# Optimization experiments

Measured on AMD Instinct MI355X. Metric: run time of the kernel, lower is better.

Reference implementation:

```python
import jax, jax.numpy as jnp
import numpy as np

V = 50257      # output vocab size
EMB = 1024     # embedding_size
HD = 1024      # decoder_hidden_size
HE = 1024      # encoder_hidden_size
L = 128        # max_src_length
B = 64         # batch_size
SCALE = 0.02


def setup_inputs() -> dict:
    key = jax.random.key(0)
    ks = jax.random.split(key, 16)
    inp = {
        "input_tensor": jax.random.randint(ks[0], (1, B), 0, V),
        "hidden": jax.random.normal(ks[1], (1, B, HD), dtype=jnp.float32),
        "encoder_outputs": jax.random.normal(ks[2], (L, B, HE), dtype=jnp.float32),
        "batch_size": B,
        # parameters
        "emb_table": jax.random.normal(ks[3], (V, EMB), dtype=jnp.float32) * SCALE,
        "attn_w": jax.random.normal(ks[4], (L, EMB + HD), dtype=jnp.float32) * SCALE,
        "attn_b": jnp.zeros((L,), dtype=jnp.float32),
        "comb_w": jax.random.normal(ks[5], (HE, EMB + HE), dtype=jnp.float32) * SCALE,
        "comb_b": jnp.zeros((HE,), dtype=jnp.float32),
        "w_ih": jax.random.normal(ks[6], (3 * HD, HE), dtype=jnp.float32) * SCALE,
        "w_hh": jax.random.normal(ks[7], (3 * HD, HD), dtype=jnp.float32) * SCALE,
        "b_ih": jnp.zeros((3 * HD,), dtype=jnp.float32),
        "b_hh": jnp.zeros((3 * HD,), dtype=jnp.float32),
        "out_w": jax.random.normal(ks[8], (V, HD), dtype=jnp.float32) * SCALE,
        "out_b": jnp.zeros((V,), dtype=jnp.float32),
    }
    return inp


def reference(input_tensor, hidden, encoder_outputs, batch_size,
              emb_table, attn_w, attn_b, comb_w, comb_b,
              w_ih, w_hh, b_ih, b_hh, out_w, out_b):
    # Embedding lookup: [1,B] -> [B,EMB] (dropout is identity at eval)
    embedded = emb_table[input_tensor[0]]
    h0 = hidden[0]  # [B,HD]

    # Bahdanau-style attention over max_src_length positions
    attn_in = jnp.concatenate([embedded, h0], axis=1)            # [B, EMB+HD]
    attn_weights = jax.nn.softmax(attn_in @ attn_w.T + attn_b, axis=1)  # [B,L]

    # context = sum_l attn[b,l] * enc[l,b,:]  (equiv of permuted bmm)
    ctx = jnp.einsum('lbe,bl->be', encoder_outputs, attn_weights)  # [B,HE]

    # attn_combine + relu
    comb = jnp.concatenate([embedded, ctx], axis=1) @ comb_w.T + comb_b
    x = jax.nn.relu(comb)  # [B,HE]

    # single-step GRU (PyTorch gate layout: r, z, n)
    gi = x @ w_ih.T + b_ih     # [B,3*HD]
    gh = h0 @ w_hh.T + b_hh    # [B,3*HD]
    i_r, i_z, i_n = jnp.split(gi, 3, axis=1)
    h_r, h_z, h_n = jnp.split(gh, 3, axis=1)
    r = jax.nn.sigmoid(i_r + h_r)
    z = jax.nn.sigmoid(i_z + h_z)
    n = jnp.tanh(i_n + r * h_n)
    h_new = (1.0 - z) * n + z * h0  # [B,HD]

    # output projection + log_softmax
    output = jax.nn.log_softmax(h_new @ out_w.T + out_b, axis=1)  # [B,V]

    return output, h_new[None], attn_weights
```

## Files before the change

kernel.cpp:

```cpp
#include <hip/hip_runtime.h>
#include <math.h>

#define V 50257
#define B 64
#define HD 1024
#define LSRC 128

typedef float v4f __attribute__((ext_vector_type(4)));
typedef __bf16 v8bf __attribute__((ext_vector_type(8)));
typedef unsigned short v8us __attribute__((ext_vector_type(8)));

__device__ inline unsigned int pk_bf2(float x, float y) {
    return (__float_as_uint(x) >> 16) | (__float_as_uint(y) & 0xffff0000u);
}
__device__ inline unsigned short bf_rne(float x) {
    unsigned int u = __float_as_uint(x);
    return (unsigned short)((u + 0x7fffu + ((u >> 16) & 1u)) >> 16);
}
__device__ inline unsigned int pk2_rne(float x, float y) {
    return (unsigned int)bf_rne(x) | ((unsigned int)bf_rne(y) << 16);
}

__global__ void k_prep(const int* __restrict__ idx, const float* __restrict__ hidden,
                       const float* __restrict__ emb, unsigned short* __restrict__ actC,
                       unsigned short* __restrict__ h0B) {
    int i = blockIdx.x * 256 + threadIdx.x;
    int b = i >> 10, k = i & 1023;
    actC[b * 2048 + k] = bf_rne(emb[(size_t)idx[b] * 1024 + k]);
    h0B[b * 1024 + k] = bf_rne(hidden[b * 1024 + k]);
}

__global__ void k_attnw(const int* __restrict__ idx, const float* __restrict__ hidden,
                        const float* __restrict__ emb, const float* __restrict__ attn_w,
                        const float* __restrict__ attn_b, float* __restrict__ attnW,
                        float* __restrict__ out2) {
    __shared__ float act[2048];
    __shared__ float sl[128];
    __shared__ float red[8];
    int b = blockIdx.x;
    int tid = threadIdx.x;
    int row = idx[b];
    for (int k = tid; k < 1024; k += 256) {
        act[k] = emb[(size_t)row * 1024 + k];
        act[1024 + k] = hidden[b * 1024 + k];
    }
    __syncthreads();
    int wave = tid >> 6, lane = tid & 63;
    for (int l = wave; l < 128; l += 4) {
        const float* wr = attn_w + (size_t)l * 2048;
        float s = 0.f;
        #pragma unroll 8
        for (int k = lane; k < 2048; k += 64) s += wr[k] * act[k];
        #pragma unroll
        for (int off = 32; off; off >>= 1) s += __shfl_xor(s, off);
        if (lane == 0) sl[l] = s + attn_b[l];
    }
    __syncthreads();
    float x = (tid < 128) ? sl[tid] : -1e30f;
    float m = x;
    #pragma unroll
    for (int off = 32; off; off >>= 1) m = fmaxf(m, __shfl_xor(m, off));
    if (lane == 0) red[wave] = m;
    __syncthreads();
    m = fmaxf(fmaxf(red[0], red[1]), fmaxf(red[2], red[3]));
    float e = (tid < 128) ? expf(x - m) : 0.f;
    float ssum = e;
    #pragma unroll
    for (int off = 32; off; off >>= 1) ssum += __shfl_xor(ssum, off);
    if (lane == 0) red[4 + wave] = ssum;
    __syncthreads();
    float stot = red[4] + red[5] + red[6] + red[7];
    if (tid < 128) {
        float w = e / stot;
        attnW[b * 128 + tid] = w;
        out2[b * 128 + tid] = w;
    }
}

__global__ void k_ctx(const float* __restrict__ attnW, const float* __restrict__ enc,
                      unsigned short* __restrict__ actC) {
    __shared__ float a[128];
    int b = blockIdx.y;
    int e = blockIdx.x * 256 + threadIdx.x;
    if (threadIdx.x < 128) a[threadIdx.x] = attnW[b * 128 + threadIdx.x];
    __syncthreads();
    float acc = 0.f;
    #pragma unroll 4
    for (int l = 0; l < 128; ++l)
        acc += a[l] * enc[((size_t)l * 64 + b) * 1024 + e];
    actC[b * 2048 + 1024 + e] = bf_rne(acc);
}

__global__ __launch_bounds__(256) void k_mm(const float* __restrict__ W,
                                            const unsigned short* __restrict__ actB,
                                            float* __restrict__ P, int M, int K, int Kc) {
    int wave = threadIdx.x >> 6, lane = threadIdx.x & 63;
    int quad = lane >> 4, r16 = lane & 15;
    int row0 = blockIdx.x * 64 + wave * 16;
    int kbase = blockIdx.y * Kc;
    const float* wr = W + (size_t)(row0 + r16) * K + kbase + quad * 8;
    const unsigned short* ab = actB + kbase + quad * 8;
    v4f acc[4] = {};
    for (int kk = 0; kk < Kc; kk += 32) {
        float4 p0 = *(const float4*)(wr + kk);
        float4 p1 = *(const float4*)(wr + kk + 4);
        union { unsigned int u[4]; v8us v; } A;
        A.u[0] = pk2_rne(p0.x, p0.y); A.u[1] = pk2_rne(p0.z, p0.w);
        A.u[2] = pk2_rne(p1.x, p1.y); A.u[3] = pk2_rne(p1.z, p1.w);
        v8bf af = __builtin_bit_cast(v8bf, A.v);
        #pragma unroll
        for (int nt = 0; nt < 4; ++nt) {
            v8us bu = *(const v8us*)(ab + (size_t)(nt * 16 + r16) * K + kk);
            v8bf bf = __builtin_bit_cast(v8bf, bu);
            acc[nt] = __builtin_amdgcn_mfma_f32_16x16x32_bf16(af, bf, acc[nt], 0, 0, 0);
        }
    }
    float* po = P + (size_t)blockIdx.y * 64 * M;
    #pragma unroll
    for (int nt = 0; nt < 4; ++nt) {
        int b = nt * 16 + r16;
        float4 val = make_float4(acc[nt][0], acc[nt][1], acc[nt][2], acc[nt][3]);
        *(float4*)(po + (size_t)b * M + row0 + quad * 4) = val;
    }
}

__global__ void k_redc(const float* __restrict__ Pc, const float* __restrict__ comb_b,
                       unsigned short* __restrict__ xB) {
    int i = blockIdx.x * 256 + threadIdx.x;
    int b = i >> 10, k = i & 1023;
    float s = comb_b[k];
    #pragma unroll
    for (int ss = 0; ss < 4; ++ss) s += Pc[((size_t)ss * 64 + b) * 1024 + k];
    s = fmaxf(s, 0.f);
    xB[b * 1024 + k] = bf_rne(s);
}

__global__ void k_gates(const float* __restrict__ Pi, const float* __restrict__ Ph,
                        const float* __restrict__ b_ih, const float* __restrict__ b_hh,
                        const float* __restrict__ hidden, float* __restrict__ out1,
                        unsigned short* __restrict__ hbf) {
    int i = blockIdx.x * 256 + threadIdx.x;
    int b = i >> 10, u = i & 1023;
    float ir = b_ih[u], iz = b_ih[1024 + u], in_ = b_ih[2048 + u];
    float hr = b_hh[u], hz = b_hh[1024 + u], hn = b_hh[2048 + u];
    #pragma unroll
    for (int s = 0; s < 4; ++s) {
        const float* pi = Pi + ((size_t)s * 64 + b) * 3072;
        const float* ph = Ph + ((size_t)s * 64 + b) * 3072;
        ir += pi[u]; iz += pi[1024 + u]; in_ += pi[2048 + u];
        hr += ph[u]; hz += ph[1024 + u]; hn += ph[2048 + u];
    }
    float r = 1.f / (1.f + __expf(-(ir + hr)));
    float z = 1.f / (1.f + __expf(-(iz + hz)));
    float n = tanhf(in_ + r * hn);
    float h0 = hidden[b * 1024 + u];
    float h = (1.f - z) * n + z * h0;
    out1[b * 1024 + u] = h;
    hbf[b * 1024 + u] = bf_rne(h);
}

__global__ __launch_bounds__(256) void k_gemm(const float* __restrict__ Wt,
                                              const unsigned short* __restrict__ hbf,
                                              const float* __restrict__ out_b,
                                              float* __restrict__ out0) {
    int wave = threadIdx.x >> 6, lane = threadIdx.x & 63;
    int quad = lane >> 4, r16 = lane & 15;
    int v0 = blockIdx.x * 128 + wave * 32;
    int va0 = min(v0 + r16, V - 1);
    int va1 = min(v0 + 16 + r16, V - 1);
    const float* wr0 = Wt + (size_t)va0 * 1024 + quad * 8;
    const float* wr1 = Wt + (size_t)va1 * 1024 + quad * 8;
    v4f acc[2][4] = {};
    for (int kk = 0; kk < 32; ++kk) {
        int kb = kk * 32;
        float4 pa0 = *(const float4*)(wr0 + kb);
        float4 pa1 = *(const float4*)(wr0 + kb + 4);
        float4 pb0 = *(const float4*)(wr1 + kb);
        float4 pb1 = *(const float4*)(wr1 + kb + 4);
        union { unsigned int u[4]; v8us v; } A0, A1;
        A0.u[0] = pk_bf2(pa0.x, pa0.y); A0.u[1] = pk_bf2(pa0.z, pa0.w);
        A0.u[2] = pk_bf2(pa1.x, pa1.y); A0.u[3] = pk_bf2(pa1.z, pa1.w);
        A1.u[0] = pk_bf2(pb0.x, pb0.y); A1.u[1] = pk_bf2(pb0.z, pb0.w);
        A1.u[2] = pk_bf2(pb1.x, pb1.y); A1.u[3] = pk_bf2(pb1.z, pb1.w);
        v8bf a0 = __builtin_bit_cast(v8bf, A0.v);
        v8bf a1 = __builtin_bit_cast(v8bf, A1.v);
        #pragma unroll
        for (int nt = 0; nt < 4; ++nt) {
            v8us bu = *(const v8us*)(hbf + (size_t)(nt * 16 + r16) * 1024 + kb + quad * 8);
            v8bf bf = __builtin_bit_cast(v8bf, bu);
            acc[0][nt] = __builtin_amdgcn_mfma_f32_16x16x32_bf16(a0, bf, acc[0][nt], 0, 0, 0);
            acc[1][nt] = __builtin_amdgcn_mfma_f32_16x16x32_bf16(a1, bf, acc[1][nt], 0, 0, 0);
        }
    }
    #pragma unroll
    for (int mt = 0; mt < 2; ++mt) {
        int vbase = v0 + mt * 16 + quad * 4;
        #pragma unroll
        for (int nt = 0; nt < 4; ++nt) {
            int b = nt * 16 + r16;
            #pragma unroll
            for (int r = 0; r < 4; ++r) {
                int v = vbase + r;
                if (v < V) out0[(size_t)b * V + v] = acc[mt][nt][r] + out_b[v];
            }
        }
    }
}

__global__ void k_lse(const float* __restrict__ out0, float* __restrict__ part) {
    int b = blockIdx.y, c = blockIdx.x;
    int tid = threadIdx.x;
    const int CH = (V + 7) / 8;
    int vs = c * CH, ve = min(vs + CH, V);
    float m = -1e30f, s = 0.f;
    for (int v = vs + tid; v < ve; v += 256) {
        float x = out0[(size_t)b * V + v];
        float nm = fmaxf(m, x);
        s = s * __expf(m - nm) + __expf(x - nm);
        m = nm;
    }
    __shared__ float sm[4], ss[4];
    int lane = tid & 63, wave = tid >> 6;
    #pragma unroll
    for (int off = 32; off; off >>= 1) {
        float om = __shfl_xor(m, off), os = __shfl_xor(s, off);
        float nm = fmaxf(m, om);
        s = s * __expf(m - nm) + os * __expf(om - nm);
        m = nm;
    }
    if (lane == 0) { sm[wave] = m; ss[wave] = s; }
    __syncthreads();
    if (tid == 0) {
        float M = sm[0], S = ss[0];
        #pragma unroll
        for (int w = 1; w < 4; ++w) {
            float nm = fmaxf(M, sm[w]);
            S = S * __expf(M - nm) + ss[w] * __expf(sm[w] - nm);
            M = nm;
        }
        part[(b * 8 + c) * 2 + 0] = M;
        part[(b * 8 + c) * 2 + 1] = S;
    }
}

__global__ void k_final(float* __restrict__ out0, const float* __restrict__ part) {
    int b = blockIdx.y;
    float M = part[b * 16 + 0], S = part[b * 16 + 1];
    #pragma unroll
    for (int c = 1; c < 8; ++c) {
        float m2 = part[(b * 8 + c) * 2], s2 = part[(b * 8 + c) * 2 + 1];
        float nm = fmaxf(M, m2);
        S = S * __expf(M - nm) + s2 * __expf(m2 - nm);
        M = nm;
    }
    float lse = M + __logf(S);
    int base = blockIdx.x * 2048 + threadIdx.x;
    #pragma unroll
    for (int j = 0; j < 8; ++j) {
        int v = base + j * 256;
        if (v < V) out0[(size_t)b * V + v] -= lse;
    }
}

extern "C" void kernel_launch(void* const* d_in, const int* in_sizes, int n_in,
                              void* d_out, int out_size, void* d_ws, size_t ws_size,
                              hipStream_t stream) {
    const int*   input_tensor = (const int*)d_in[0];
    const float* hidden  = (const float*)d_in[1];
    const float* enc     = (const float*)d_in[2];
    const float* emb     = (const float*)d_in[4];
    const float* attn_w  = (const float*)d_in[5];
    const float* attn_b  = (const float*)d_in[6];
    const float* comb_w  = (const float*)d_in[7];
    const float* comb_b  = (const float*)d_in[8];
    const float* w_ih    = (const float*)d_in[9];
    const float* w_hh    = (const float*)d_in[10];
    const float* b_ih    = (const float*)d_in[11];
    const float* b_hh    = (const float*)d_in[12];
    const float* out_w   = (const float*)d_in[13];
    const float* out_b   = (const float*)d_in[14];

    float* out0 = (float*)d_out;
    float* out1 = out0 + (size_t)B * V;
    float* out2 = out1 + B * HD;

    float* ws    = (float*)d_ws;
    float* attnW = ws;
    float* part  = ws + 8192;
    float* Pc    = ws + 9216;
    unsigned short* actC = (unsigned short*)(ws + 271360);
    unsigned short* h0B  = (unsigned short*)(ws + 336896);
    unsigned short* xB   = (unsigned short*)(ws + 369664);
    unsigned short* hbf  = (unsigned short*)(ws + 402432);

    float* Pi = out0;
    float* Ph = out0 + 4 * 64 * 3072;

    k_prep<<<256, 256, 0, stream>>>(input_tensor, hidden, emb, actC, h0B);
    k_attnw<<<64, 256, 0, stream>>>(input_tensor, hidden, emb, attn_w, attn_b, attnW, out2);
    k_ctx<<<dim3(4, 64), 256, 0, stream>>>(attnW, enc, actC);
    k_mm<<<dim3(16, 4), 256, 0, stream>>>(comb_w, actC, Pc, 1024, 2048, 512);
    k_mm<<<dim3(48, 4), 256, 0, stream>>>(w_hh, h0B, Ph, 3072, 1024, 256);
    k_redc<<<256, 256, 0, stream>>>(Pc, comb_b, xB);
    k_mm<<<dim3(48, 4), 256, 0, stream>>>(w_ih, xB, Pi, 3072, 1024, 256);
    k_gates<<<256, 256, 0, stream>>>(Pi, Ph, b_ih, b_hh, hidden, out1, hbf);
    k_gemm<<<393, 256, 0, stream>>>(out_w, hbf, out_b, out0);
    k_lse<<<dim3(8, 64), 256, 0, stream>>>(out0, part);
    k_final<<<dim3(25, 64), 256, 0, stream>>>(out0, part);
}
```

Before: 615.7 us.

## Fuse LSE into output GEMM, MFMA attention scores, merge comb/hh GEMMs

The attention score projection moves from a scalar dot-product kernel to the bf16 MFMA split-K GEMM, and softmax is fused with the context reduction. The comb_w and w_hh GEMMs are merged into one launch. The output GEMM now uses 64-row blocks (786 of them), switches from truncating to round-to-nearest bf16 conversion of the weights, and computes per-block online max/sum partials, so the separate pass that reread the full logits is dropped. The goal is fewer launches and less logits traffic, at the cost of halving per-block weight reuse in the output GEMM and extra rounding work.

Result: faster. 541.3 us (-12.1%).

```diff
diff --git a/kernel.cpp b/kernel.cpp
--- a/kernel.cpp
+++ b/kernel.cpp
@@ -5,14 +5,12 @@
 #define B 64
 #define HD 1024
 #define LSRC 128
+#define NBLK 786
 
 typedef float v4f __attribute__((ext_vector_type(4)));
 typedef __bf16 v8bf __attribute__((ext_vector_type(8)));
 typedef unsigned short v8us __attribute__((ext_vector_type(8)));
 
-__device__ inline unsigned int pk_bf2(float x, float y) {
-    return (__float_as_uint(x) >> 16) | (__float_as_uint(y) & 0xffff0000u);
-}
 __device__ inline unsigned short bf_rne(float x) {
     unsigned int u = __float_as_uint(x);
     return (unsigned short)((u + 0x7fffu + ((u >> 16) & 1u)) >> 16);
@@ -22,84 +20,30 @@
 }
 
 __global__ void k_prep(const int* __restrict__ idx, const float* __restrict__ hidden,
-                       const float* __restrict__ emb, unsigned short* __restrict__ actC,
-                       unsigned short* __restrict__ h0B) {
+                       const float* __restrict__ emb, unsigned short* __restrict__ catB,
+                       unsigned short* __restrict__ actC) {
     int i = blockIdx.x * 256 + threadIdx.x;
-    int b = i >> 10, k = i & 1023;
-    actC[b * 2048 + k] = bf_rne(emb[(size_t)idx[b] * 1024 + k]);
-    h0B[b * 1024 + k] = bf_rne(hidden[b * 1024 + k]);
-}
-
-__global__ void k_attnw(const int* __restrict__ idx, const float* __restrict__ hidden,
-                        const float* __restrict__ emb, const float* __restrict__ attn_w,
-                        const float* __restrict__ attn_b, float* __restrict__ attnW,
-                        float* __restrict__ out2) {
-    __shared__ float act[2048];
-    __shared__ float sl[128];
-    __shared__ float red[8];
-    int b = blockIdx.x;
-    int tid = threadIdx.x;
-    int row = idx[b];
-    for (int k = tid; k < 1024; k += 256) {
-        act[k] = emb[(size_t)row * 1024 + k];
-        act[1024 + k] = hidden[b * 1024 + k];
-    }
-    __syncthreads();
+    int b = i >> 11, k = i & 2047;
+    unsigned short v;
+    if (k < 1024) {
+        v = bf_rne(emb[(size_t)idx[b] * 1024 + k]);
+        actC[b * 2048 + k] = v;
+    } else {
+        v = bf_rne(hidden[b * 1024 + (k - 1024)]);
+    }
+    catB[b * 2048 + k] = v;
+}
+
+__device__ __forceinline__ void mm_core(const float* __restrict__ W,
+                                        const unsigned short* __restrict__ act, int as_,
+                                        float* __restrict__ P, int M, int K, int Kc,
+                                        int mx, int ks, int tid) {
     int wave = tid >> 6, lane = tid & 63;
-    for (int l = wave; l < 128; l += 4) {
-        const float* wr = attn_w + (size_t)l * 2048;
-        float s = 0.f;
-        #pragma unroll 8
-        for (int k = lane; k < 2048; k += 64) s += wr[k] * act[k];
-        #pragma unroll
-        for (int off = 32; off; off >>= 1) s += __shfl_xor(s, off);
-        if (lane == 0) sl[l] = s + attn_b[l];
-    }
-    __syncthreads();
-    float x = (tid < 128) ? sl[tid] : -1e30f;
-    float m = x;
-    #pragma unroll
-    for (int off = 32; off; off >>= 1) m = fmaxf(m, __shfl_xor(m, off));
-    if (lane == 0) red[wave] = m;
-    __syncthreads();
-    m = fmaxf(fmaxf(red[0], red[1]), fmaxf(red[2], red[3]));
-    float e = (tid < 128) ? expf(x - m) : 0.f;
-    float ssum = e;
-    #pragma unroll
-    for (int off = 32; off; off >>= 1) ssum += __shfl_xor(ssum, off);
-    if (lane == 0) red[4 + wave] = ssum;
-    __syncthreads();
-    float stot = red[4] + red[5] + red[6] + red[7];
-    if (tid < 128) {
-        float w = e / stot;
-        attnW[b * 128 + tid] = w;
-        out2[b * 128 + tid] = w;
-    }
-}
-
-__global__ void k_ctx(const float* __restrict__ attnW, const float* __restrict__ enc,
-                      unsigned short* __restrict__ actC) {
-    __shared__ float a[128];
-    int b = blockIdx.y;
-    int e = blockIdx.x * 256 + threadIdx.x;
-    if (threadIdx.x < 128) a[threadIdx.x] = attnW[b * 128 + threadIdx.x];
-    __syncthreads();
-    float acc = 0.f;
-    #pragma unroll 4
-    for (int l = 0; l < 128; ++l)
-        acc += a[l] * enc[((size_t)l * 64 + b) * 1024 + e];
-    actC[b * 2048 + 1024 + e] = bf_rne(acc);
-}
-
-__global__ __launch_bounds__(256) void k_mm(const float* __restrict__ W,
-                                            const unsigned short* __restrict__ actB,
-                                            float* __restrict__ P, int M, int K, int Kc) {
-    int wave = threadIdx.x >> 6, lane = threadIdx.x & 63;
     int quad = lane >> 4, r16 = lane & 15;
-    int row0 = blockIdx.x * 64 + wave * 16;
-    int kbase = blockIdx.y * Kc;
+    int row0 = mx * 64 + wave * 16;
+    int kbase = ks * Kc;
     const float* wr = W + (size_t)(row0 + r16) * K + kbase + quad * 8;
-    const unsigned short* ab = actB + kbase + quad * 8;
+    const unsigned short* ab = act + kbase + quad * 8;
     v4f acc[4] = {};
     for (int kk = 0; kk < Kc; kk += 32) {
         float4 p0 = *(const float4*)(wr + kk);
@@ -110,18 +54,78 @@
         v8bf af = __builtin_bit_cast(v8bf, A.v);
         #pragma unroll
         for (int nt = 0; nt < 4; ++nt) {
-            v8us bu = *(const v8us*)(ab + (size_t)(nt * 16 + r16) * K + kk);
+            v8us bu = *(const v8us*)(ab + (size_t)(nt * 16 + r16) * as_ + kk);
             v8bf bf = __builtin_bit_cast(v8bf, bu);
             acc[nt] = __builtin_amdgcn_mfma_f32_16x16x32_bf16(af, bf, acc[nt], 0, 0, 0);
         }
     }
-    float* po = P + (size_t)blockIdx.y * 64 * M;
+    float* po = P + (size_t)ks * 64 * M;
     #pragma unroll
     for (int nt = 0; nt < 4; ++nt) {
         int b = nt * 16 + r16;
         float4 val = make_float4(acc[nt][0], acc[nt][1], acc[nt][2], acc[nt][3]);
         *(float4*)(po + (size_t)b * M + row0 + quad * 4) = val;
     }
+}
+
+__global__ __launch_bounds__(256) void k_mm(const float* __restrict__ W,
+                                            const unsigned short* __restrict__ act,
+                                            float* __restrict__ P, int M, int K, int Kc,
+                                            int as_) {
+    mm_core(W, act, as_, P, M, K, Kc, blockIdx.x, blockIdx.y, threadIdx.x);
+}
+
+__global__ __launch_bounds__(256) void k_mm2(const float* __restrict__ Wc,
+                                             const unsigned short* __restrict__ actC,
+                                             float* __restrict__ Pc,
+                                             const float* __restrict__ Wh,
+                                             const unsigned short* __restrict__ h0B,
+                                             float* __restrict__ Ph) {
+    int bx = blockIdx.x;
+    if (bx < 16) mm_core(Wc, actC, 2048, Pc, 1024, 2048, 512, bx, blockIdx.y, threadIdx.x);
+    else         mm_core(Wh, h0B, 2048, Ph, 3072, 1024, 256, bx - 16, blockIdx.y, threadIdx.x);
+}
+
+__global__ void k_ctxs(const float* __restrict__ Pa, const float* __restrict__ attn_b,
+                       const float* __restrict__ enc, unsigned short* __restrict__ actC,
+                       float* __restrict__ out2) {
+    __shared__ float a_sh[128];
+    __shared__ float red[8];
+    int b = blockIdx.y, tid = threadIdx.x;
+    int lane = tid & 63, wave = tid >> 6;
+    float x = -1e30f;
+    if (tid < 128) {
+        x = attn_b[tid];
+        #pragma unroll
+        for (int ks = 0; ks < 4; ++ks) x += Pa[(ks * 64 + b) * 128 + tid];
+    }
+    float m = x;
+    #pragma unroll
+    for (int off = 32; off; off >>= 1) m = fmaxf(m, __shfl_xor(m, off));
+    if (lane == 0) red[wave] = m;
+    __syncthreads();
+    m = fmaxf(fmaxf(red[0], red[1]), fmaxf(red[2], red[3]));
+    float e = (tid < 128) ? __expf(x - m) : 0.f;
+    float ssum = e;
+    #pragma unroll
+    for (int off = 32; off; off >>= 1) ssum += __shfl_xor(ssum, off);
+    if (lane == 0) red[4 + wave] = ssum;
+    __syncthreads();
+    float stot = red[4] + red[5] + red[6] + red[7];
+    if (tid < 128) {
+        float w = e / stot;
+        a_sh[tid] = w;
+        if (blockIdx.x == 0) out2[b * 128 + tid] = w;
+    }
+    __syncthreads();
+    int e0 = blockIdx.x * 256 + tid;
+    float acc0 = 0.f, acc1 = 0.f;
+    #pragma unroll 8
+    for (int l = 0; l < 128; l += 2) {
+        acc0 += a_sh[l]     * enc[((size_t)(l * 64) + b) * 1024 + e0];
+        acc1 += a_sh[l + 1] * enc[((size_t)((l + 1) * 64) + b) * 1024 + e0];
+    }
+    actC[b * 2048 + 1024 + e0] = bf_rne(acc0 + acc1);
 }
 
 __global__ void k_redc(const float* __restrict__ Pc, const float* __restrict__ comb_b,
@@ -162,65 +166,82 @@
 __global__ __launch_bounds__(256) void k_gemm(const float* __restrict__ Wt,
                                               const unsigned short* __restrict__ hbf,
                                               const float* __restrict__ out_b,
-                                              float* __restrict__ out0) {
-    int wave = threadIdx.x >> 6, lane = threadIdx.x & 63;
+                                              float* __restrict__ out0,
+                                              float* __restrict__ m_part,
+                                              float* __restrict__ s_part) {
+    __shared__ float sm[4][64], ss[4][64];
+    int tid = threadIdx.x;
+    int wave = tid >> 6, lane = tid & 63;
     int quad = lane >> 4, r16 = lane & 15;
-    int v0 = blockIdx.x * 128 + wave * 32;
-    int va0 = min(v0 + r16, V - 1);
-    int va1 = min(v0 + 16 + r16, V - 1);
-    const float* wr0 = Wt + (size_t)va0 * 1024 + quad * 8;
-    const float* wr1 = Wt + (size_t)va1 * 1024 + quad * 8;
-    v4f acc[2][4] = {};
-    for (int kk = 0; kk < 32; ++kk) {
-        int kb = kk * 32;
-        float4 pa0 = *(const float4*)(wr0 + kb);
-        float4 pa1 = *(const float4*)(wr0 + kb + 4);
-        float4 pb0 = *(const float4*)(wr1 + kb);
-        float4 pb1 = *(const float4*)(wr1 + kb + 4);
-        union { unsigned int u[4]; v8us v; } A0, A1;
-        A0.u[0] = pk_bf2(pa0.x, pa0.y); A0.u[1] = pk_bf2(pa0.z, pa0.w);
-        A0.u[2] = pk_bf2(pa1.x, pa1.y); A0.u[3] = pk_bf2(pa1.z, pa1.w);
-        A1.u[0] = pk_bf2(pb0.x, pb0.y); A1.u[1] = pk_bf2(pb0.z, pb0.w);
-        A1.u[2] = pk_bf2(pb1.x, pb1.y); A1.u[3] = pk_bf2(pb1.z, pb1.w);
-        v8bf a0 = __builtin_bit_cast(v8bf, A0.v);
-        v8bf a1 = __builtin_bit_cast(v8bf, A1.v);
+    int v0 = blockIdx.x * 64 + wave * 16;
+    int va = min(v0 + r16, V - 1);
+    const float* wr = Wt + (size_t)va * 1024 + quad * 8;
+    const unsigned short* ab = hbf + quad * 8;
+    v4f acc[4] = {};
+    for (int kk = 0; kk < 1024; kk += 32) {
+        float4 p0 = *(const float4*)(wr + kk);
+        float4 p1 = *(const float4*)(wr + kk + 4);
+        union { unsigned int u[4]; v8us v; } A;
+        A.u[0] = pk2_rne(p0.x, p0.y); A.u[1] = pk2_rne(p0.z, p0.w);
+        A.u[2] = pk2_rne(p1.x, p1.y); A.u[3] = pk2_rne(p1.z, p1.w);
+        v8bf af = __builtin_bit_cast(v8bf, A.v);
         #pragma unroll
         for (int nt = 0; nt < 4; ++nt) {
-            v8us bu = *(const v8us*)(hbf + (size_t)(nt * 16 + r16) * 1024 + kb + quad * 8);
+            v8us bu = *(const v8us*)(ab + (size_t)(nt * 16 + r16) * 1024 + kk);
             v8bf bf = __builtin_bit_cast(v8bf, bu);
-            acc[0][nt] = __builtin_amdgcn_mfma_f32_16x16x32_bf16(a0, bf, acc[0][nt], 0, 0, 0);
-            acc[1][nt] = __builtin_amdgcn_mfma_f32_16x16x32_bf16(a1, bf, acc[1][nt], 0, 0, 0);
-        }
-    }
-    #pragma unroll
-    for (int mt = 0; mt < 2; ++mt) {
-        int vbase = v0 + mt * 16 + quad * 4;
-        #pragma unroll
-        for (int nt = 0; nt < 4; ++nt) {
-            int b = nt * 16 + r16;
-            #pragma unroll
-            for (int r = 0; r < 4; ++r) {
-                int v = vbase + r;
-                if (v < V) out0[(size_t)b * V + v] = acc[mt][nt][r] + out_b[v];
+            acc[nt] = __builtin_amdgcn_mfma_f32_16x16x32_bf16(af, bf, acc[nt], 0, 0, 0);
+        }
+    }
+    #pragma unroll
+    for (int nt = 0; nt < 4; ++nt) {
+        int b = nt * 16 + r16;
+        float lm = -1e30f, lsum = 0.f;
+        #pragma unroll
+        for (int r = 0; r < 4; ++r) {
+            int v = v0 + quad * 4 + r;
+            if (v < V) {
+                float x = acc[nt][r] + out_b[v];
+                out0[(size_t)b * V + v] = x;
+                float nm = fmaxf(lm, x);
+                lsum = lsum * __expf(lm - nm) + __expf(x - nm);
+                lm = nm;
             }
         }
-    }
-}
-
-__global__ void k_lse(const float* __restrict__ out0, float* __restrict__ part) {
-    int b = blockIdx.y, c = blockIdx.x;
-    int tid = threadIdx.x;
-    const int CH = (V + 7) / 8;
-    int vs = c * CH, ve = min(vs + CH, V);
+        #pragma unroll
+        for (int off = 16; off <= 32; off <<= 1) {
+            float om = __shfl_xor(lm, off), os = __shfl_xor(lsum, off);
+            float nm = fmaxf(lm, om);
+            lsum = lsum * __expf(lm - nm) + os * __expf(om - nm);
+            lm = nm;
+        }
+        if (quad == 0) { sm[wave][b] = lm; ss[wave][b] = lsum; }
+    }
+    __syncthreads();
+    if (tid < 64) {
+        float M2 = sm[0][tid], S2 = ss[0][tid];
+        #pragma unroll
+        for (int w = 1; w < 4; ++w) {
+            float nm = fmaxf(M2, sm[w][tid]);
+            S2 = S2 * __expf(M2 - nm) + ss[w][tid] * __expf(sm[w][tid] - nm);
+            M2 = nm;
+        }
+        m_part[(size_t)tid * NBLK + blockIdx.x] = M2;
+        s_part[(size_t)tid * NBLK + blockIdx.x] = S2;
+    }
+}
+
+__global__ void k_comb(const float* __restrict__ m_part, const float* __restrict__ s_part,
+                       float* __restrict__ lse) {
+    __shared__ float sm[4], ss[4];
+    int b = blockIdx.x, tid = threadIdx.x;
+    int lane = tid & 63, wave = tid >> 6;
     float m = -1e30f, s = 0.f;
-    for (int v = vs + tid; v < ve; v += 256) {
-        float x = out0[(size_t)b * V + v];
-        float nm = fmaxf(m, x);
-        s = s * __expf(m - nm) + __expf(x - nm);
+    for (int i = tid; i < NBLK; i += 256) {
+        float om = m_part[(size_t)b * NBLK + i], os = s_part[(size_t)b * NBLK + i];
+        float nm = fmaxf(m, om);
+        s = s * __expf(m - nm) + os * __expf(om - nm);
         m = nm;
     }
-    __shared__ float sm[4], ss[4];
-    int lane = tid & 63, wave = tid >> 6;
     #pragma unroll
     for (int off = 32; off; off >>= 1) {
         float om = __shfl_xor(m, off), os = __shfl_xor(s, off);
@@ -238,27 +259,18 @@
             S = S * __expf(M - nm) + ss[w] * __expf(sm[w] - nm);
             M = nm;
         }
-        part[(b * 8 + c) * 2 + 0] = M;
-        part[(b * 8 + c) * 2 + 1] = S;
-    }
-}
-
-__global__ void k_final(float* __restrict__ out0, const float* __restrict__ part) {
+        lse[b] = M + __logf(S);
+    }
+}
+
+__global__ void k_final(float* __restrict__ out0, const float* __restrict__ lse) {
     int b = blockIdx.y;
-    float M = part[b * 16 + 0], S = part[b * 16 + 1];
-    #pragma unroll
-    for (int c = 1; c < 8; ++c) {
-        float m2 = part[(b * 8 + c) * 2], s2 = part[(b * 8 + c) * 2 + 1];
-        float nm = fmaxf(M, m2);
-        S = S * __expf(M - nm) + s2 * __expf(m2 - nm);
-        M = nm;
-    }
-    float lse = M + __logf(S);
+    float l = lse[b];
     int base = blockIdx.x * 2048 + threadIdx.x;
     #pragma unroll
     for (int j = 0; j < 8; ++j) {
         int v = base + j * 256;
-        if (v < V) out0[(size_t)b * V + v] -= lse;
+        if (v < V) out0[(size_t)b * V + v] -= l;
     }
 }
 
@@ -284,27 +296,28 @@
     float* out1 = out0 + (size_t)B * V;
     float* out2 = out1 + B * HD;
 
-    float* ws    = (float*)d_ws;
-    float* attnW = ws;
-    float* part  = ws + 8192;
-    float* Pc    = ws + 9216;
-    unsigned short* actC = (unsigned short*)(ws + 271360);
-    unsigned short* h0B  = (unsigned short*)(ws + 336896);
-    unsigned short* xB   = (unsigned short*)(ws + 369664);
-    unsigned short* hbf  = (unsigned short*)(ws + 402432);
+    float* ws = (float*)d_ws;
+    float* Pa     = ws;
+    float* Pc     = ws + 32768;
+    float* lse    = ws + 294912;
+    float* m_part = ws + 294976;
+    float* s_part = ws + 345280;
+    unsigned short* catB = (unsigned short*)(ws + 395584);
+    unsigned short* actC = (unsigned short*)(ws + 461120);
+    unsigned short* xB   = (unsigned short*)(ws + 526656);
+    unsigned short* hbf  = (unsigned short*)(ws + 543040);
 
     float* Pi = out0;
     float* Ph = out0 + 4 * 64 * 3072;
 
-    k_prep<<<256, 256, 0, stream>>>(input_tensor, hidden, emb, actC, h0B);
-    k_attnw<<<64, 256, 0, stream>>>(input_tensor, hidden, emb, attn_w, attn_b, attnW, out2);
-    k_ctx<<<dim3(4, 64), 256, 0, stream>>>(attnW, enc, actC);
-    k_mm<<<dim3(16, 4), 256, 0, stream>>>(comb_w, actC, Pc, 1024, 2048, 512);
-    k_mm<<<dim3(48, 4), 256, 0, stream>>>(w_hh, h0B, Ph, 3072, 1024, 256);
+    k_prep<<<512, 256, 0, stream>>>(input_tensor, hidden, emb, catB, actC);
+    k_mm<<<dim3(2, 4), 256, 0, stream>>>(attn_w, catB, Pa, 128, 2048, 512, 2048);
+    k_ctxs<<<dim3(4, 64), 256, 0, stream>>>(Pa, attn_b, enc, actC, out2);
+    k_mm2<<<dim3(64, 4), 256, 0, stream>>>(comb_w, actC, Pc, w_hh, catB + 1024, Ph);
     k_redc<<<256, 256, 0, stream>>>(Pc, comb_b, xB);
-    k_mm<<<dim3(48, 4), 256, 0, stream>>>(w_ih, xB, Pi, 3072, 1024, 256);
+    k_mm<<<dim3(48, 4), 256, 0, stream>>>(w_ih, xB, Pi, 3072, 1024, 256, 1024);
     k_gates<<<256, 256, 0, stream>>>(Pi, Ph, b_ih, b_hh, hidden, out1, hbf);
-    k_gemm<<<393, 256, 0, stream>>>(out_w, hbf, out_b, out0);
-    k_lse<<<dim3(8, 64), 256, 0, stream>>>(out0, part);
-    k_final<<<dim3(25, 64), 256, 0, stream>>>(out0, part);
-}
+    k_gemm<<<NBLK, 256, 0, stream>>>(out_w, hbf, out_b, out0, m_part, s_part);
+    k_comb<<<64, 256, 0, stream>>>(m_part, s_part, lse);
+    k_final<<<dim3(25, 64), 256, 0, stream>>>(out0, lse);
+}
```
